# Kernel tuning notes

Measured on AMD Instinct MI355X. Metric: run time of the kernel, lower is better.

## Reference

```python
import jax, jax.numpy as jnp
import numpy as np

B, S, D, H, N = 2, 2048, 768, 12, 128  # batch, seq_len, d_model, n_heads, num_segments
EPS_LN = 1e-5


def _layer_norm(x, g, b):
    m = x.mean(-1, keepdims=True)
    v = ((x - m) ** 2).mean(-1, keepdims=True)
    return (x - m) / jnp.sqrt(v + EPS_LN) * g + b


def _mha(q, k, v, Wqkv, bqkv, Wo, bo, n_heads):
    """torch.nn.MultiheadAttention (batch_first), returns (out, head-averaged attn)."""
    d = q.shape[-1]
    dh = d // n_heads
    Wq, Wk, Wv = jnp.split(Wqkv, 3, axis=0)
    bq, bk, bv = jnp.split(bqkv, 3)
    qh = (q @ Wq.T + bq).reshape(q.shape[0], q.shape[1], n_heads, dh)
    kh = (k @ Wk.T + bk).reshape(k.shape[0], k.shape[1], n_heads, dh)
    vh = (v @ Wv.T + bv).reshape(v.shape[0], v.shape[1], n_heads, dh)
    scores = jnp.einsum('bqhd,bkhd->bhqk', qh, kh) / jnp.sqrt(jnp.asarray(dh, q.dtype))
    attn = jax.nn.softmax(scores, axis=-1)                      # [B,H,Sq,Sk]
    out = jnp.einsum('bhqk,bkhd->bqhd', attn, vh).reshape(q.shape[0], q.shape[1], d)
    return out @ Wo.T + bo, attn.mean(axis=1)                   # attn avg over heads


def _aggregate(x, w, seg):  # per-batch: weighted mean of tokens into N segments
    num = jax.ops.segment_sum(w[:, None] * x, seg, num_segments=N)
    den = jax.ops.segment_sum(w, seg, num_segments=N)
    return num / (den[:, None] + 1e-8)


def setup_inputs() -> dict:
    key = jax.random.key(0)
    ks = jax.random.split(key, 16)
    s = 0.02
    inp = {
        'hidden_states': jax.random.normal(ks[0], (B, S, D), jnp.float32),
        'token_to_segment': jnp.sort(jax.random.randint(ks[1], (B, S), 0, N), axis=-1),
        # token_attention (shared for node-level self-attn in the adjacency=None branch)
        'Wqkv_t': jax.random.normal(ks[2], (3 * D, D), jnp.float32) * s,
        'bqkv_t': jnp.zeros((3 * D,), jnp.float32),
        'Wo_t': jax.random.normal(ks[3], (D, D), jnp.float32) * s,
        'bo_t': jnp.zeros((D,), jnp.float32),
        # cross_attention
        'Wqkv_c': jax.random.normal(ks[4], (3 * D, D), jnp.float32) * s,
        'bqkv_c': jnp.zeros((3 * D,), jnp.float32),
        'Wo_c': jax.random.normal(ks[5], (D, D), jnp.float32) * s,
        'bo_c': jnp.zeros((D,), jnp.float32),
        # layer norms
        'g_tok': jnp.ones((D,), jnp.float32),
        'b_tok': jnp.zeros((D,), jnp.float32),
        'g_node': jnp.ones((D,), jnp.float32),
        'b_node': jnp.zeros((D,), jnp.float32),
        # output projection
        'W_out': jax.random.normal(ks[6], (D, D), jnp.float32) * s,
        'b_out': jnp.zeros((D,), jnp.float32),
    }
    return inp


def reference(hidden_states, token_to_segment, Wqkv_t, bqkv_t, Wo_t, bo_t,
              Wqkv_c, bqkv_c, Wo_c, bo_c, g_tok, b_tok, g_node, b_node,
              W_out, b_out):
    hs = hidden_states
    # token-level self-attention + residual norm
    tok_attn_out, tok_attn = _mha(hs, hs, hs, Wqkv_t, bqkv_t, Wo_t, bo_t, H)
    token_output = _layer_norm(hs + tok_attn_out, g_tok, b_tok)
    # token -> node attention-weighted scatter aggregation
    w = tok_attn.mean(axis=1)  # [B,S] attention received per token
    node_emb = jax.vmap(_aggregate)(token_output, w, token_to_segment)  # [B,N,D]
    # node-level self-attention (reuses token_attention weights; adjacency=None path)
    node_out, node_attn = _mha(node_emb, node_emb, node_emb, Wqkv_t, bqkv_t, Wo_t, bo_t, H)
    node_emb = _layer_norm(node_emb + node_out, g_node, b_node)
    # cross-attention: tokens attend to nodes
    cross_out, cross_w = _mha(token_output, node_emb, node_emb, Wqkv_c, bqkv_c, Wo_c, bo_c, H)
    token_output = token_output + cross_out
    # node -> token gather + additive combine
    gathered = jnp.take_along_axis(node_emb, token_to_segment[:, :, None], axis=1)  # [B,S,D]
    enhanced = token_output + gathered
    output = enhanced @ W_out.T + b_out
    return output, node_emb, tok_attn, node_attn, cross_w
```

## Files before the change

### kernel.cpp

```cpp
#include <hip/hip_runtime.h>
#include <cstdint>

#define B_ 2
#define S_ 2048
#define D_ 768
#define H_ 12
#define DH_ 64
#define N_ 128

typedef unsigned short u16;
typedef unsigned int u32;
typedef __attribute__((ext_vector_type(8))) short short8;
typedef __attribute__((ext_vector_type(4))) float f32x4;

#define MFMA16(a, b, c) __builtin_amdgcn_mfma_f32_16x16x32_bf16(a, b, c, 0, 0, 0)

__device__ inline u16 f2bf(float f) {
  union { float f; u32 u; } v; v.f = f;
  u32 r = v.u + 0x7FFFu + ((v.u >> 16) & 1u);
  return (u16)(r >> 16);
}
__device__ inline u32 pk2(float a, float b) {
  return (u32)f2bf(a) | ((u32)f2bf(b) << 16);
}
__device__ inline float wredmax(float v) {
  #pragma unroll
  for (int o = 32; o > 0; o >>= 1) v = fmaxf(v, __shfl_down(v, o));
  return v;
}
__device__ inline float wredsum(float v) {
  #pragma unroll
  for (int o = 32; o > 0; o >>= 1) v += __shfl_down(v, o);
  return v;
}
__device__ inline void async_lds16(const u16* g, u16* l) {
  __builtin_amdgcn_global_load_lds((const __attribute__((address_space(1))) void*)g,
                                   (__attribute__((address_space(3))) void*)l, 16, 0, 0);
}

__global__ void conv_bf16(const float* __restrict__ in, u16* __restrict__ outp, int n8) {
  int i = blockIdx.x * 256 + threadIdx.x;
  if (i >= n8) return;
  const float4* p = (const float4*)(in + (size_t)i * 8);
  float4 a = p[0], b = p[1];
  uint4 u;
  u.x = pk2(a.x, a.y); u.y = pk2(a.z, a.w); u.z = pk2(b.x, b.y); u.w = pk2(b.z, b.w);
  *(uint4*)(outp + (size_t)i * 8) = u;
}

template <int OUT_BF16>
__global__ __launch_bounds__(256) void gemm_bf16(
    const u16* __restrict__ A, int lda,
    const u16* __restrict__ W, int ldb,
    const float* __restrict__ bias,
    void* __restrict__ Cout, int ldc, int K) {
  __shared__ u16 As[128 * 32];
  __shared__ u16 Ws[128 * 32];
  const int tid = threadIdx.x;
  const int m0 = blockIdx.y * 128, n0 = blockIdx.x * 128;
  const int w = tid >> 6, lane = tid & 63;
  const int msub = (w & 1) * 64, nsub = (w >> 1) * 64;
  const int lrow = lane & 15, quad = lane >> 4;
  const int e0 = tid * 8;
  const int r0 = e0 >> 5, c0 = e0 & 31;
  const int e1 = e0 + 2048;
  const int r1 = e1 >> 5, c1 = e1 & 31;
  const u16* Ag0 = A + (size_t)(m0 + r0) * lda + c0;
  const u16* Ag1 = A + (size_t)(m0 + r1) * lda + c1;
  const u16* Wg0 = W + (size_t)(n0 + r0) * ldb + c0;
  const u16* Wg1 = W + (size_t)(n0 + r1) * ldb + c1;
  u16* AsB0 = As + (w << 9);
  u16* AsB1 = As + 2048 + (w << 9);
  u16* WsB0 = Ws + (w << 9);
  u16* WsB1 = Ws + 2048 + (w << 9);
  f32x4 zero = {0.f, 0.f, 0.f, 0.f};
  f32x4 acc[4][4];
  #pragma unroll
  for (int i = 0; i < 4; i++)
    #pragma unroll
    for (int j = 0; j < 4; j++) acc[i][j] = zero;
  for (int k0 = 0; k0 < K; k0 += 32) {
    __syncthreads();
    async_lds16(Ag0 + k0, AsB0);
    async_lds16(Ag1 + k0, AsB1);
    async_lds16(Wg0 + k0, WsB0);
    async_lds16(Wg1 + k0, WsB1);
    __syncthreads();
    short8 af[4], bf[4];
    #pragma unroll
    for (int i = 0; i < 4; i++)
      af[i] = *(const short8*)(As + (msub + i * 16 + lrow) * 32 + quad * 8);
    #pragma unroll
    for (int j = 0; j < 4; j++)
      bf[j] = *(const short8*)(Ws + (nsub + j * 16 + lrow) * 32 + quad * 8);
    #pragma unroll
    for (int i = 0; i < 4; i++)
      #pragma unroll
      for (int j = 0; j < 4; j++)
        acc[i][j] = MFMA16(af[i], bf[j], acc[i][j]);
  }
  #pragma unroll
  for (int i = 0; i < 4; i++) {
    #pragma unroll
    for (int j = 0; j < 4; j++) {
      int col = n0 + nsub + j * 16 + lrow;
      float bv = bias ? bias[col] : 0.f;
      #pragma unroll
      for (int r = 0; r < 4; r++) {
        int row = m0 + msub + i * 16 + quad * 4 + r;
        float val = acc[i][j][r] + bv;
        if (OUT_BF16) ((u16*)Cout)[(size_t)row * ldc + col] = f2bf(val);
        else ((float*)Cout)[(size_t)row * ldc + col] = val;
      }
    }
  }
}

__global__ __launch_bounds__(256) void transpose_v(const u16* __restrict__ qkv, u16* __restrict__ VT) {
  __shared__ u16 t[64][72];
  const int z = blockIdx.y, b = z / 12, h = z - b * 12;
  const int s0 = blockIdx.x * 64;
  const int tid = threadIdx.x;
  {
    int r = tid >> 2, dp = (tid & 3) * 16;
    const u16* src = qkv + (size_t)b * 2048 * 2304 + (size_t)(s0 + r) * 2304 + 1536 + h * 64 + dp;
    *(uint4*)&t[r][dp] = *(const uint4*)src;
    *(uint4*)&t[r][dp + 8] = *(const uint4*)(src + 8);
  }
  __syncthreads();
  int d = tid >> 2, sp = (tid & 3) * 16;
  u16 vals[16];
  #pragma unroll
  for (int i = 0; i < 16; i++) vals[i] = t[sp + i][d];
  u16* dst = VT + ((size_t)z * 64 + d) * 2048 + s0 + sp;
  *(uint4*)dst = *(uint4*)&vals[0];
  *(uint4*)(dst + 8) = *(uint4*)&vals[8];
}

__global__ __launch_bounds__(512, 2) void fused_tok_attn(
    const u16* __restrict__ qkv, const u16* __restrict__ VT,
    float* __restrict__ am, u16* __restrict__ attnout) {
  __shared__ u16 pbuf[8 * 16 * 40];
  __shared__ float lred[8][16];
  __shared__ float obuf[8][16][66];
  const int tid = threadIdx.x;
  const int w = tid >> 6, lane = tid & 63;
  const int lrow = lane & 15, quad = lane >> 4;
  const int blk = blockIdx.x;
  const int b = blk >> 7, q0 = (blk & 127) << 4;
  const u16* qp = qkv + (size_t)b * 2048 * 2304;
  const u16* kp = qp + 768;
  const int strip = w * 256;
  float* amrow = am + (size_t)b * 2048 * 2048 + (size_t)q0 * 2048;
  u16* ob = attnout + (size_t)b * 2048 * 768 + (size_t)q0 * 768;
  u16* pb = pbuf + w * 640;
  const float c12 = 1.f / 12.f;
  f32x4 zero = {0.f, 0.f, 0.f, 0.f};
  float amreg[4][16];
  #pragma unroll
  for (int r = 0; r < 4; r++)
    #pragma unroll
    for (int c = 0; c < 16; c++) amreg[r][c] = 0.f;
  for (int h = 0; h < 12; h++) {
    const u16* qh = qp + (size_t)(q0 + lrow) * 2304 + h * 64 + quad * 8;
    short8 qf0 = *(const short8*)qh;
    short8 qf1 = *(const short8*)(qh + 32);
    f32x4 pex[16];
    float lsum[4] = {0.f, 0.f, 0.f, 0.f};
    #pragma unroll
    for (int t = 0; t < 16; t++) {
      const u16* kh = kp + (size_t)(strip + t * 16 + lrow) * 2304 + h * 64 + quad * 8;
      short8 kf0 = *(const short8*)kh;
      short8 kf1 = *(const short8*)(kh + 32);
      f32x4 sv = zero;
      sv = MFMA16(qf0, kf0, sv);
      sv = MFMA16(qf1, kf1, sv);
      f32x4 pe;
      #pragma unroll
      for (int r = 0; r < 4; r++) pe[r] = __expf(sv[r] * 0.125f);
      #pragma unroll
      for (int r = 0; r < 4; r++) lsum[r] += pe[r];
      pex[t] = pe;
    }
    #pragma unroll
    for (int o = 1; o < 16; o <<= 1)
      #pragma unroll
      for (int r = 0; r < 4; r++) lsum[r] += __shfl_xor(lsum[r], o);
    if (lrow == 0) {
      #pragma unroll
      for (int r = 0; r < 4; r++) lred[w][quad * 4 + r] = lsum[r];
    }
    __syncthreads();
    float invl[4];
    #pragma unroll
    for (int r = 0; r < 4; r++) {
      float s = 0.f;
      #pragma unroll
      for (int w2 = 0; w2 < 8; w2++) s += lred[w2][quad * 4 + r];
      invl[r] = 1.f / s;
    }
    f32x4 oacc[4];
    #pragma unroll
    for (int j = 0; j < 4; j++) oacc[j] = zero;
    const u16* vtp = VT + (size_t)(b * 12 + h) * 64 * 2048;
    #pragma unroll
    for (int c = 0; c < 8; c++) {
      const int cbase = strip + c * 32;
      short8 vf[4];
      #pragma unroll
      for (int j = 0; j < 4; j++)
        vf[j] = *(const short8*)(vtp + (size_t)(j * 16 + lrow) * 2048 + cbase + quad * 8);
      #pragma unroll
      for (int t2 = 0; t2 < 2; t2++) {
        #pragma unroll
        for (int r = 0; r < 4; r++) {
          float p = pex[c * 2 + t2][r] * invl[r];
          amreg[r][c * 2 + t2] += p;
          pb[(quad * 4 + r) * 40 + t2 * 16 + lrow] = f2bf(p);
        }
      }
      asm volatile("s_waitcnt lgkmcnt(0)" ::: "memory");
      short8 pf = *(const short8*)(pb + lrow * 40 + quad * 8);
      #pragma unroll
      for (int j = 0; j < 4; j++) oacc[j] = MFMA16(pf, vf[j], oacc[j]);
      asm volatile("s_waitcnt lgkmcnt(0)" ::: "memory");
    }
    #pragma unroll
    for (int j = 0; j < 4; j++)
      #pragma unroll
      for (int r = 0; r < 4; r++)
        obuf[w][quad * 4 + r][j * 16 + lrow] = oacc[j][r];
    __syncthreads();
    #pragma unroll
    for (int ee = 0; ee < 2; ee++) {
      int e = tid + ee * 512;
      int row = e >> 6, col = e & 63;
      float s = 0.f;
      #pragma unroll
      for (int w2 = 0; w2 < 8; w2++) s += obuf[w2][row][col];
      ob[(size_t)row * 768 + h * 64 + col] = f2bf(s);
    }
    __syncthreads();
  }
  #pragma unroll
  for (int r = 0; r < 4; r++) {
    float* ar = amrow + (size_t)(quad * 4 + r) * 2048;
    #pragma unroll
    for (int c = 0; c < 8; c++) {
      ar[strip + c * 32 + lrow] = amreg[r][c * 2] * c12;
      ar[strip + c * 32 + 16 + lrow] = amreg[r][c * 2 + 1] * c12;
    }
  }
}

__global__ __launch_bounds__(256) void qk_mfma(
    const u16* __restrict__ Q, int ldq, long qbs,
    const u16* __restrict__ Kp, int ldk, long kbs,
    float* __restrict__ S, long szs, int Sk, int nh, float scale) {
  __shared__ u16 Qs[128 * 72];
  __shared__ u16 Ks[128 * 72];
  const int tid = threadIdx.x;
  const int z = blockIdx.z, bb = z / nh, h = z - bb * nh;
  const u16* qp = Q + (size_t)bb * qbs + h * 64;
  const u16* kp = Kp + (size_t)bb * kbs + h * 64;
  float* sp = S + (size_t)z * szs;
  const int m0 = blockIdx.y * 128, n0 = blockIdx.x * 128;
  const int w = tid >> 6, lane = tid & 63;
  const int msub = (w & 1) * 64, nsub = (w >> 1) * 64;
  const int lrow = lane & 15, quad = lane >> 4;
  const int srow = tid >> 1, shalf = tid & 1;
  {
    const uint4* qg = (const uint4*)(qp + (size_t)(m0 + srow) * ldq + shalf * 32);
    const uint4* kg = (const uint4*)(kp + (size_t)(n0 + srow) * ldk + shalf * 32);
    uint4* qd = (uint4*)(Qs + srow * 72 + shalf * 32);
    uint4* kd = (uint4*)(Ks + srow * 72 + shalf * 32);
    #pragma unroll
    for (int u = 0; u < 4; u++) { qd[u] = qg[u]; kd[u] = kg[u]; }
  }
  __syncthreads();
  f32x4 zero = {0.f, 0.f, 0.f, 0.f};
  f32x4 acc[4][4];
  #pragma unroll
  for (int i = 0; i < 4; i++)
    #pragma unroll
    for (int j = 0; j < 4; j++) acc[i][j] = zero;
  #pragma unroll
  for (int ks = 0; ks < 2; ks++) {
    short8 af[4], bf[4];
    #pragma unroll
    for (int i = 0; i < 4; i++)
      af[i] = *(const short8*)(Qs + (msub + i * 16 + lrow) * 72 + ks * 32 + quad * 8);
    #pragma unroll
    for (int j = 0; j < 4; j++)
      bf[j] = *(const short8*)(Ks + (nsub + j * 16 + lrow) * 72 + ks * 32 + quad * 8);
    #pragma unroll
    for (int i = 0; i < 4; i++)
      #pragma unroll
      for (int j = 0; j < 4; j++)
        acc[i][j] = MFMA16(af[i], bf[j], acc[i][j]);
  }
  #pragma unroll
  for (int i = 0; i < 4; i++)
    #pragma unroll
    for (int j = 0; j < 4; j++) {
      int col = n0 + nsub + j * 16 + lrow;
      #pragma unroll
      for (int r = 0; r < 4; r++) {
        int row = m0 + msub + i * 16 + quad * 4 + r;
        sp[(size_t)row * Sk + col] = acc[i][j][r] * scale;
      }
    }
}

__global__ __launch_bounds__(128) void softmax_small(
    float* __restrict__ Sc, float* __restrict__ wout, int Sq) {
  const int q = blockIdx.x, b = blockIdx.y, tid = threadIdx.x;
  const int w = tid >> 6, lane = tid & 63;
  __shared__ float red[2];
  float am = 0.f;
  const size_t plane = (size_t)Sq * 128;
  for (int h = 0; h < 12; h++) {
    const int z = b * 12 + h;
    float* row = Sc + (size_t)z * plane + (size_t)q * 128;
    float v = row[tid];
    float m = wredmax(v);
    if (lane == 0) red[w] = m;
    __syncthreads();
    m = fmaxf(red[0], red[1]);
    float e = __expf(v - m);
    float s = wredsum(e);
    __syncthreads();
    if (lane == 0) red[w] = s;
    __syncthreads();
    float p = e / (red[0] + red[1]);
    ((u16*)(Sc + (size_t)z * plane))[(size_t)q * 256 + tid] = f2bf(p);
    am += p;
    __syncthreads();
  }
  wout[((size_t)b * Sq + q) * 128 + tid] = am * (1.f / 12.f);
}

__global__ __launch_bounds__(256) void pv_small(
    const u16* __restrict__ Pb, long pzs,
    const u16* __restrict__ KVb, int ldv, long vbs, int vhoff,
    u16* __restrict__ Outb, long obs) {
  __shared__ u16 Ps[128 * 40];
  __shared__ u16 Vs[64 * 40];
  const int tid = threadIdx.x;
  const int z = blockIdx.y, b = z / 12, h = z - b * 12;
  const u16* Pp = Pb + (size_t)z * pzs;
  const u16* Vp = KVb + (size_t)b * vbs + vhoff + h * 64;
  u16* Op = Outb + (size_t)b * obs + h * 64;
  const int m0 = blockIdx.x * 128;
  const int w = tid >> 6, lane = tid & 63;
  const int msub = w * 32;
  const int lrow = lane & 15, quad = lane >> 4;
  const int srow = tid >> 1, shalf = tid & 1;
  const int vk = tid >> 3, vn = (tid & 7) * 8;
  f32x4 zero = {0.f, 0.f, 0.f, 0.f};
  f32x4 acc[2][4];
  #pragma unroll
  for (int i = 0; i < 2; i++)
    #pragma unroll
    for (int j = 0; j < 4; j++) acc[i][j] = zero;
  #pragma unroll
  for (int k0 = 0; k0 < 128; k0 += 32) {
    uint4 pa = *(const uint4*)(Pp + (size_t)(m0 + srow) * 256 + k0 + shalf * 16);
    uint4 pb2 = *(const uint4*)(Pp + (size_t)(m0 + srow) * 256 + k0 + shalf * 16 + 8);
    uint4 vv = *(const uint4*)(Vp + (size_t)(k0 + vk) * ldv + vn);
    __syncthreads();
    *(uint4*)(Ps + srow * 40 + shalf * 16) = pa;
    *(uint4*)(Ps + srow * 40 + shalf * 16 + 8) = pb2;
    const u16* vs = (const u16*)&vv;
    #pragma unroll
    for (int u = 0; u < 8; u++) Vs[(vn + u) * 40 + vk] = vs[u];
    __syncthreads();
    short8 af[2], bf[4];
    #pragma unroll
    for (int i = 0; i < 2; i++)
      af[i] = *(const short8*)(Ps + (msub + i * 16 + lrow) * 40 + quad * 8);
    #pragma unroll
    for (int j = 0; j < 4; j++)
      bf[j] = *(const short8*)(Vs + (j * 16 + lrow) * 40 + quad * 8);
    #pragma unroll
    for (int i = 0; i < 2; i++)
      #pragma unroll
      for (int j = 0; j < 4; j++)
        acc[i][j] = MFMA16(af[i], bf[j], acc[i][j]);
  }
  #pragma unroll
  for (int i = 0; i < 2; i++)
    #pragma unroll
    for (int j = 0; j < 4; j++) {
      int col = j * 16 + lrow;
      #pragma unroll
      for (int r = 0; r < 4; r++) {
        int row = m0 + msub + i * 16 + quad * 4 + r;
        Op[(size_t)row * D_ + col] = f2bf(acc[i][j][r]);
      }
    }
}

__global__ void ln_kernel(const float* __restrict__ x1, const float* __restrict__ x2,
                          const float* __restrict__ g, const float* __restrict__ bt,
                          float* __restrict__ outp, u16* __restrict__ outbf) {
  const int row = blockIdx.x;
  const int tid = threadIdx.x;
  __shared__ float red[8];
  float v[3];
  #pragma unroll
  for (int j = 0; j < 3; j++) {
    int c = tid + j * 256;
    v[j] = x1[(size_t)row * D_ + c] + x2[(size_t)row * D_ + c];
  }
  float s = v[0] + v[1] + v[2];
  s = wredsum(s);
  int wid = tid >> 6, lane = tid & 63;
  if (lane == 0) red[wid] = s;
  __syncthreads();
  float mean = (red[0] + red[1] + red[2] + red[3]) / 768.f;
  float d0 = v[0] - mean, d1 = v[1] - mean, d2 = v[2] - mean;
  float q = d0 * d0 + d1 * d1 + d2 * d2;
  q = wredsum(q);
  if (lane == 0) red[4 + wid] = q;
  __syncthreads();
  float var = (red[4] + red[5] + red[6] + red[7]) / 768.f;
  float inv = rsqrtf(var + 1e-5f);
  #pragma unroll
  for (int j = 0; j < 3; j++) {
    int c = tid + j * 256;
    float val = (v[j] - mean) * inv * g[c] + bt[c];
    outp[(size_t)row * D_ + c] = val;
    if (outbf) outbf[(size_t)row * D_ + c] = f2bf(val);
  }
}

__global__ void colmean_part(const float* __restrict__ ta, float* __restrict__ part) {
  int b = blockIdx.y, z = blockIdx.z;
  int k = blockIdx.x * 256 + threadIdx.x;
  const float* p = ta + (size_t)b * S_ * S_ + (size_t)z * 256 * S_ + k;
  float s = 0.f;
  #pragma unroll 8
  for (int q = 0; q < 256; q++) s += p[(size_t)q * S_];
  part[((size_t)z * B_ + b) * S_ + k] = s;
}

__global__ void colmean_final(const float* __restrict__ part, float* __restrict__ w) {
  int b = blockIdx.y;
  int k = blockIdx.x * 256 + threadIdx.x;
  float s = 0.f;
  #pragma unroll
  for (int z = 0; z < 8; z++) s += part[((size_t)z * B_ + b) * S_ + k];
  w[b * S_ + k] = s * (1.f / (float)S_);
}

__global__ void aggregate_kernel(const float* __restrict__ x, const float* __restrict__ w,
                                 const int* __restrict__ seg, float* __restrict__ outp,
                                 u16* __restrict__ outbf) {
  const int b = blockIdx.y, n = blockIdx.x;
  const int* sg = seg + b * S_;
  int l = 0, rr = S_;
  while (l < rr) { int mid = (l + rr) >> 1; if (sg[mid] < n) l = mid + 1; else rr = mid; }
  const int lo = l;
  rr = S_;
  while (l < rr) { int mid = (l + rr) >> 1; if (sg[mid] < n + 1) l = mid + 1; else rr = mid; }
  const int hi = l;
  const int tid = threadIdx.x;
  float acc[3] = {0.f, 0.f, 0.f};
  float den = 0.f;
  for (int s = lo; s < hi; s++) {
    float ww = w[b * S_ + s];
    den += ww;
    const float* xr = x + (size_t)(b * S_ + s) * D_;
    #pragma unroll
    for (int j = 0; j < 3; j++) acc[j] += ww * xr[tid + j * 256];
  }
  float invd = 1.f / (den + 1e-8f);
  size_t ro = (size_t)(b * N_ + n) * D_;
  #pragma unroll
  for (int j = 0; j < 3; j++) {
    float val = acc[j] * invd;
    outp[ro + tid + j * 256] = val;
    outbf[ro + tid + j * 256] = f2bf(val);
  }
}

__global__ void enhanced_kernel(const float* __restrict__ tokout, const float* __restrict__ crossp,
                                const float* __restrict__ nodeemb, const int* __restrict__ seg,
                                u16* __restrict__ outbf) {
  int g8 = blockIdx.x * 256 + threadIdx.x;
  int bs = g8 / 96, d0 = (g8 - bs * 96) * 8;
  int b = bs >> 11;
  int n = seg[bs];
  const float* t = tokout + (size_t)bs * D_ + d0;
  const float* cp = crossp + (size_t)bs * D_ + d0;
  const float* ne = nodeemb + (size_t)(b * N_ + n) * D_ + d0;
  float4 a0 = *(const float4*)t, a1 = *(const float4*)(t + 4);
  float4 b0 = *(const float4*)cp, b1 = *(const float4*)(cp + 4);
  float4 c0 = *(const float4*)ne, c1 = *(const float4*)(ne + 4);
  uint4 u;
  u.x = pk2(a0.x + b0.x + c0.x, a0.y + b0.y + c0.y);
  u.y = pk2(a0.z + b0.z + c0.z, a0.w + b0.w + c0.w);
  u.z = pk2(a1.x + b1.x + c1.x, a1.y + b1.y + c1.y);
  u.w = pk2(a1.z + b1.z + c1.z, a1.w + b1.w + c1.w);
  *(uint4*)(outbf + (size_t)g8 * 8) = u;
}

extern "C" void kernel_launch(void* const* d_in, const int* in_sizes, int n_in,
                              void* d_out, int out_size, void* d_ws, size_t ws_size,
                              hipStream_t stream) {
  const float* hs     = (const float*)d_in[0];
  const int*   t2s    = (const int*)d_in[1];
  const float* Wqkv_t = (const float*)d_in[2];
  const float* bqkv_t = (const float*)d_in[3];
  const float* Wo_t   = (const float*)d_in[4];
  const float* bo_t   = (const float*)d_in[5];
  const float* Wqkv_c = (const float*)d_in[6];
  const float* bqkv_c = (const float*)d_in[7];
  const float* Wo_c   = (const float*)d_in[8];
  const float* bo_c   = (const float*)d_in[9];
  const float* g_tok  = (const float*)d_in[10];
  const float* b_tok  = (const float*)d_in[11];
  const float* g_node = (const float*)d_in[12];
  const float* b_node = (const float*)d_in[13];
  const float* W_out  = (const float*)d_in[14];
  const float* b_out  = (const float*)d_in[15];

  float* ws = (float*)d_ws;
  u16*   qkvbf       = (u16*)ws;
  u16*   enh_bf      = (u16*)ws;
  u16*   crossqbf    = (u16*)(ws + 1572864);
  u16*   crossattn_bf= (u16*)(ws + 3145728);
  float* R1 = ws + 4718592;
  u16*   hs_bf   = (u16*)R1;
  u16*   wqkvt1  = (u16*)(R1 + 1572864);
  u16*   VT      = (u16*)R1;
  float* projbuf = R1;
  float* Snode   = R1;
  u16*   wqkvt2  = (u16*)(R1 + 4000000);
  u16*   wot     = (u16*)(R1 + 6291456);
  u16*   wqkvc   = (u16*)R1;
  u16*   woc     = (u16*)(R1 + 6291456);
  u16*   wout    = (u16*)(R1 + 6586368);
  float* Scross  = R1;
  float* crossproj = R1;
  float* R2 = ws + 13107200;
  u16*   attnout_bf = (u16*)R2;
  u16*   tokout_bf  = (u16*)R2;
  float* wvec       = R2 + 1572864;
  float* colpart    = R2 + 1576960;
  float* nodepre    = R2 + 1609728;
  float* nodeproj   = R2 + 1806336;
  u16*   nodepre_bf = (u16*)(R2 + 2002944);
  u16*   nodeattn_bf= (u16*)(R2 + 2101248);
  u16*   nodeemb_bf = (u16*)(R2 + 2199552);
  u16*   nodeqkvbf  = (u16*)(R2 + 2297856);
  u16*   crosskvbf  = (u16*)(R2 + 2592768);
  float* tokout = ws + 16252928;

  float* outp       = (float*)d_out;
  float* o_output   = outp;
  float* o_nodeemb  = outp + 3145728;
  float* o_tokattn  = o_nodeemb + 196608;
  float* o_nodeattn = o_tokattn + 8388608;
  float* o_crossw   = o_nodeattn + 32768;

  conv_bf16<<<1536, 256, 0, stream>>>(hs, hs_bf, 393216);
  conv_bf16<<<864, 256, 0, stream>>>(Wqkv_t, wqkvt1, 221184);
  gemm_bf16<1><<<dim3(18, 32), 256, 0, stream>>>(hs_bf, 768, wqkvt1, 768, bqkv_t, qkvbf, 2304, 768);

  transpose_v<<<dim3(32, 24), 256, 0, stream>>>(qkvbf, VT);
  fused_tok_attn<<<256, 512, 0, stream>>>(qkvbf, VT, o_tokattn, attnout_bf);

  conv_bf16<<<288, 256, 0, stream>>>(Wo_t, wot, 73728);
  gemm_bf16<0><<<dim3(6, 32), 256, 0, stream>>>(attnout_bf, 768, wot, 768, bo_t, projbuf, 768, 768);
  ln_kernel<<<4096, 256, 0, stream>>>(hs, projbuf, g_tok, b_tok, tokout, tokout_bf);

  colmean_part<<<dim3(8, 2, 8), 256, 0, stream>>>(o_tokattn, colpart);
  colmean_final<<<dim3(8, 2), 256, 0, stream>>>(colpart, wvec);
  aggregate_kernel<<<dim3(128, 2), 256, 0, stream>>>(tokout, wvec, t2s, nodepre, nodepre_bf);
  conv_bf16<<<864, 256, 0, stream>>>(Wqkv_t, wqkvt2, 221184);
  gemm_bf16<1><<<dim3(18, 2), 256, 0, stream>>>(nodepre_bf, 768, wqkvt2, 768, bqkv_t, nodeqkvbf, 2304, 768);
  qk_mfma<<<dim3(1, 1, 24), 256, 0, stream>>>(
      nodeqkvbf, 2304, (long)128 * 2304, nodeqkvbf + 768, 2304, (long)128 * 2304,
      Snode, 16384, 128, 12, 0.125f);
  softmax_small<<<dim3(128, 2), 128, 0, stream>>>(Snode, o_nodeattn, 128);
  pv_small<<<dim3(1, 24), 256, 0, stream>>>(
      (const u16*)Snode, 32768, nodeqkvbf, 2304, (long)128 * 2304, 1536,
      nodeattn_bf, (long)128 * 768);
  gemm_bf16<0><<<dim3(6, 2), 256, 0, stream>>>(nodeattn_bf, 768, wot, 768, bo_t, nodeproj, 768, 768);
  ln_kernel<<<256, 256, 0, stream>>>(nodepre, nodeproj, g_node, b_node, o_nodeemb, nodeemb_bf);

  conv_bf16<<<864, 256, 0, stream>>>(Wqkv_c, wqkvc, 221184);
  conv_bf16<<<288, 256, 0, stream>>>(Wo_c, woc, 73728);
  conv_bf16<<<288, 256, 0, stream>>>(W_out, wout, 73728);
  gemm_bf16<1><<<dim3(6, 32), 256, 0, stream>>>(tokout_bf, 768, wqkvc, 768, bqkv_c, crossqbf, 768, 768);
  gemm_bf16<1><<<dim3(12, 2), 256, 0, stream>>>(nodeemb_bf, 768, wqkvc + 768 * 768, 768, bqkv_c + 768,
                                                crosskvbf, 1536, 768);

  qk_mfma<<<dim3(1, 16, 24), 256, 0, stream>>>(
      crossqbf, 768, (long)2048 * 768, crosskvbf, 1536, (long)128 * 1536,
      Scross, 262144, 128, 12, 0.125f);
  softmax_small<<<dim3(2048, 2), 128, 0, stream>>>(Scross, o_crossw, 2048);
  pv_small<<<dim3(16, 24), 256, 0, stream>>>(
      (const u16*)Scross, 524288, crosskvbf, 1536, (long)128 * 1536, 768,
      crossattn_bf, (long)2048 * 768);

  gemm_bf16<0><<<dim3(6, 32), 256, 0, stream>>>(crossattn_bf, 768, woc, 768, bo_c, crossproj, 768, 768);
  enhanced_kernel<<<1536, 256, 0, stream>>>(tokout, crossproj, o_nodeemb, t2s, enh_bf);
  gemm_bf16<0><<<dim3(6, 32), 256, 0, stream>>>(enh_bf, 768, wout, 768, b_out, o_output, 768, 768);
}
```

Measured before the change: 626.1 us.

## Stage unnormalized probabilities in LDS via transposed QK MFMA in token attention

Swaps the MFMA operand order so each lane holds scores for one query row. Unnormalized exp values go straight to an enlarged per-wave LDS buffer as bf16, which drops the 16 f32x4 register array and the per-chunk LDS round trips. Softmax normalization moves to the output accumulator. The head-averaged attention is accumulated from the bf16 LDS values and stored with vectorized float4 writes. Register pressure and synchronization go down, at the cost of more LDS and head-averaged attention values that carry bf16 rounding.

```diff
diff --git a/kernel.cpp b/kernel.cpp
--- a/kernel.cpp
+++ b/kernel.cpp
@@ -10,6 +10,7 @@
 
 typedef unsigned short u16;
 typedef unsigned int u32;
+typedef unsigned long long u64;
 typedef __attribute__((ext_vector_type(8))) short short8;
 typedef __attribute__((ext_vector_type(4))) float f32x4;
 
@@ -22,6 +23,10 @@
 }
 __device__ inline u32 pk2(float a, float b) {
   return (u32)f2bf(a) | ((u32)f2bf(b) << 16);
+}
+__device__ inline float bf2f(u16 h) {
+  union { u32 u; float f; } v; v.u = ((u32)h) << 16;
+  return v.f;
 }
 __device__ inline float wredmax(float v) {
   #pragma unroll
@@ -140,7 +145,7 @@
 __global__ __launch_bounds__(512, 2) void fused_tok_attn(
     const u16* __restrict__ qkv, const u16* __restrict__ VT,
     float* __restrict__ am, u16* __restrict__ attnout) {
-  __shared__ u16 pbuf[8 * 16 * 40];
+  __shared__ u16 pbuf[8][16][264];
   __shared__ float lred[8][16];
   __shared__ float obuf[8][16][66];
   const int tid = threadIdx.x;
@@ -151,53 +156,55 @@
   const u16* qp = qkv + (size_t)b * 2048 * 2304;
   const u16* kp = qp + 768;
   const int strip = w * 256;
-  float* amrow = am + (size_t)b * 2048 * 2048 + (size_t)q0 * 2048;
+  float* amrow = am + (size_t)b * 2048 * 2048 + (size_t)(q0 + lrow) * 2048 + strip;
   u16* ob = attnout + (size_t)b * 2048 * 768 + (size_t)q0 * 768;
-  u16* pb = pbuf + w * 640;
+  u16* pb = &pbuf[w][0][0];
   const float c12 = 1.f / 12.f;
   f32x4 zero = {0.f, 0.f, 0.f, 0.f};
-  float amreg[4][16];
-  #pragma unroll
-  for (int r = 0; r < 4; r++)
-    #pragma unroll
-    for (int c = 0; c < 16; c++) amreg[r][c] = 0.f;
+  float amreg[8][8];
+  #pragma unroll
+  for (int c = 0; c < 8; c++)
+    #pragma unroll
+    for (int e = 0; e < 8; e++) amreg[c][e] = 0.f;
   for (int h = 0; h < 12; h++) {
     const u16* qh = qp + (size_t)(q0 + lrow) * 2304 + h * 64 + quad * 8;
     short8 qf0 = *(const short8*)qh;
     short8 qf1 = *(const short8*)(qh + 32);
-    f32x4 pex[16];
-    float lsum[4] = {0.f, 0.f, 0.f, 0.f};
+    float lsum = 0.f;
     #pragma unroll
     for (int t = 0; t < 16; t++) {
       const u16* kh = kp + (size_t)(strip + t * 16 + lrow) * 2304 + h * 64 + quad * 8;
       short8 kf0 = *(const short8*)kh;
       short8 kf1 = *(const short8*)(kh + 32);
       f32x4 sv = zero;
-      sv = MFMA16(qf0, kf0, sv);
-      sv = MFMA16(qf1, kf1, sv);
-      f32x4 pe;
-      #pragma unroll
-      for (int r = 0; r < 4; r++) pe[r] = __expf(sv[r] * 0.125f);
-      #pragma unroll
-      for (int r = 0; r < 4; r++) lsum[r] += pe[r];
-      pex[t] = pe;
+      sv = MFMA16(kf0, qf0, sv);
+      sv = MFMA16(kf1, qf1, sv);
+      float pe0 = __expf(sv[0] * 0.125f);
+      float pe1 = __expf(sv[1] * 0.125f);
+      float pe2 = __expf(sv[2] * 0.125f);
+      float pe3 = __expf(sv[3] * 0.125f);
+      lsum += (pe0 + pe1) + (pe2 + pe3);
+      u32 w0 = pk2(pe0, pe1), w1 = pk2(pe2, pe3);
+      *(u64*)(pb + lrow * 264 + t * 16 + quad * 4) = (u64)w0 | ((u64)w1 << 32);
     }
-    #pragma unroll
-    for (int o = 1; o < 16; o <<= 1)
-      #pragma unroll
-      for (int r = 0; r < 4; r++) lsum[r] += __shfl_xor(lsum[r], o);
-    if (lrow == 0) {
-      #pragma unroll
-      for (int r = 0; r < 4; r++) lred[w][quad * 4 + r] = lsum[r];
-    }
-    __syncthreads();
-    float invl[4];
-    #pragma unroll
-    for (int r = 0; r < 4; r++) {
+    lsum += __shfl_xor(lsum, 16);
+    lsum += __shfl_xor(lsum, 32);
+    if (lane < 16) lred[w][lane] = lsum;
+    __syncthreads();
+    float invq;
+    float inv4[4];
+    {
       float s = 0.f;
       #pragma unroll
-      for (int w2 = 0; w2 < 8; w2++) s += lred[w2][quad * 4 + r];
-      invl[r] = 1.f / s;
+      for (int w2 = 0; w2 < 8; w2++) s += lred[w2][lrow];
+      invq = 1.f / s;
+      #pragma unroll
+      for (int r = 0; r < 4; r++) {
+        float sr = 0.f;
+        #pragma unroll
+        for (int w2 = 0; w2 < 8; w2++) sr += lred[w2][quad * 4 + r];
+        inv4[r] = 1.f / sr;
+      }
     }
     f32x4 oacc[4];
     #pragma unroll
@@ -205,36 +212,29 @@
     const u16* vtp = VT + (size_t)(b * 12 + h) * 64 * 2048;
     #pragma unroll
     for (int c = 0; c < 8; c++) {
-      const int cbase = strip + c * 32;
+      short8 pf = *(const short8*)(pb + lrow * 264 + c * 32 + quad * 8);
       short8 vf[4];
       #pragma unroll
       for (int j = 0; j < 4; j++)
-        vf[j] = *(const short8*)(vtp + (size_t)(j * 16 + lrow) * 2048 + cbase + quad * 8);
-      #pragma unroll
-      for (int t2 = 0; t2 < 2; t2++) {
-        #pragma unroll
-        for (int r = 0; r < 4; r++) {
-          float p = pex[c * 2 + t2][r] * invl[r];
-          amreg[r][c * 2 + t2] += p;
-          pb[(quad * 4 + r) * 40 + t2 * 16 + lrow] = f2bf(p);
-        }
-      }
-      asm volatile("s_waitcnt lgkmcnt(0)" ::: "memory");
-      short8 pf = *(const short8*)(pb + lrow * 40 + quad * 8);
+        vf[j] = *(const short8*)(vtp + (size_t)(j * 16 + lrow) * 2048 + strip + c * 32 + quad * 8);
       #pragma unroll
       for (int j = 0; j < 4; j++) oacc[j] = MFMA16(pf, vf[j], oacc[j]);
-      asm volatile("s_waitcnt lgkmcnt(0)" ::: "memory");
+      #pragma unroll
+      for (int e = 0; e < 8; e++)
+        amreg[c][e] += bf2f((u16)pf[e]) * invq;
     }
+    asm volatile("s_waitcnt lgkmcnt(0)" ::: "memory");
+    __builtin_amdgcn_sched_barrier(0);
     #pragma unroll
     for (int j = 0; j < 4; j++)
       #pragma unroll
       for (int r = 0; r < 4; r++)
-        obuf[w][quad * 4 + r][j * 16 + lrow] = oacc[j][r];
+        obuf[w][quad * 4 + r][j * 16 + lrow] = oacc[j][r] * inv4[r];
     __syncthreads();
     #pragma unroll
     for (int ee = 0; ee < 2; ee++) {
-      int e = tid + ee * 512;
-      int row = e >> 6, col = e & 63;
+      int e2 = tid + ee * 512;
+      int row = e2 >> 6, col = e2 & 63;
       float s = 0.f;
       #pragma unroll
       for (int w2 = 0; w2 < 8; w2++) s += obuf[w2][row][col];
@@ -243,13 +243,11 @@
     __syncthreads();
   }
   #pragma unroll
-  for (int r = 0; r < 4; r++) {
-    float* ar = amrow + (size_t)(quad * 4 + r) * 2048;
-    #pragma unroll
-    for (int c = 0; c < 8; c++) {
-      ar[strip + c * 32 + lrow] = amreg[r][c * 2] * c12;
-      ar[strip + c * 32 + 16 + lrow] = amreg[r][c * 2 + 1] * c12;
-    }
+  for (int c = 0; c < 8; c++) {
+    float4 v0 = {amreg[c][0] * c12, amreg[c][1] * c12, amreg[c][2] * c12, amreg[c][3] * c12};
+    float4 v1 = {amreg[c][4] * c12, amreg[c][5] * c12, amreg[c][6] * c12, amreg[c][7] * c12};
+    *(float4*)(amrow + c * 32 + quad * 8) = v0;
+    *(float4*)(amrow + c * 32 + quad * 8 + 4) = v1;
   }
 }
 
```

Measured after the change: 626.1 us. About the same (+0.0%).
